# Performance work log

Measured on AMD Instinct MI355X. Metric: run time of the kernel, lower is better.

## Reference

```python
import jax, jax.numpy as jnp
import numpy as np

N_QUBITS = 10
DIM = 2 ** N_QUBITS
N_TOKENS = 32
LAYERS = 2
DEGREE = 3
VOCAB = 32000
EMB = 512
N_PARAMS = 4 * N_QUBITS * LAYERS      # angles per token circuit
N_PARAMS_FF = 4 * N_QUBITS            # quantum feedforward (1 layer)
BATCH = 32


def _ry(state, wire, theta, n):
    # state: [B, 2**n] complex64; theta: [B] float32. RY = [[c,-s],[s,c]], c=cos(th/2)
    st = state.reshape(-1, 2 ** wire, 2, 2 ** (n - wire - 1))
    c = jnp.cos(theta / 2)[:, None, None]
    s = jnp.sin(theta / 2)[:, None, None]
    a, b = st[:, :, 0, :], st[:, :, 1, :]
    st = jnp.stack([c * a - s * b, s * a + c * b], axis=2)
    return st.reshape(-1, 2 ** n)


def _crx(state, ctrl, tgt, theta, n):
    # controlled-RX: apply RX=[[c,-i s],[-i s,c]] on tgt where ctrl bit == 1
    lo, hi = (ctrl, tgt) if ctrl < tgt else (tgt, ctrl)
    st = state.reshape(-1, 2 ** lo, 2, 2 ** (hi - lo - 1), 2, 2 ** (n - hi - 1))
    caxis = 2 if ctrl < tgt else 4
    taxis = 4 if ctrl < tgt else 2
    c = jnp.cos(theta / 2).reshape(-1, 1, 1, 1, 1, 1)
    s = jnp.sin(theta / 2).reshape(-1, 1, 1, 1, 1, 1)
    c0 = jax.lax.index_in_dim(st, 0, caxis, keepdims=True)
    c1 = jax.lax.index_in_dim(st, 1, caxis, keepdims=True)
    a = jax.lax.index_in_dim(c1, 0, taxis, keepdims=True)
    b = jax.lax.index_in_dim(c1, 1, taxis, keepdims=True)
    na = c * a - 1j * s * b
    nb = -1j * s * a + c * b
    c1 = jnp.concatenate([na, nb], axis=taxis)
    st = jnp.concatenate([c0, c1], axis=caxis)
    return st.reshape(-1, 2 ** n)


def _ansatz14(state, params, n, layers):
    # gate order of ansatz 14 (arXiv:1905.10876); params: [B, 4*n*layers]
    idx = 0
    for _ in range(layers):
        for i in range(n):
            state = _ry(state, i, params[:, idx], n); idx += 1
        for i in range(n - 1, -1, -1):
            state = _crx(state, i, (i + 1) % n, params[:, idx], n); idx += 1
        for i in range(n):
            state = _ry(state, i, params[:, idx], n); idx += 1
        for i in [n - 1] + list(range(n - 1)):
            state = _crx(state, i, (i - 1) % n, params[:, idx], n); idx += 1
    return state


def _measure_xyz(state, n):
    # expectation of X,Y,Z on every wire; output [B, 3*n] ordered [x..., y..., z...]
    B = state.shape[0]
    xs, ys, zs = [], [], []
    for w in range(n):
        st = state.reshape(B, 2 ** w, 2, 2 ** (n - w - 1))
        a, b = st[:, :, 0, :], st[:, :, 1, :]
        z = jnp.sum(jnp.conj(a) * b, axis=(1, 2))
        xs.append(2.0 * jnp.real(z))
        ys.append(2.0 * jnp.imag(z))
        zs.append(jnp.sum(jnp.real(a * jnp.conj(a)) - jnp.real(b * jnp.conj(b)), axis=(1, 2)))
    return jnp.stack(xs + ys + zs, axis=1)


def _forward(x, emb, w_ang, b_ang, qsvt_coeffs, lcu_re, lcu_im, qff_params, w1, b1, w2, b2):
    B, T = x.shape
    lcu = (lcu_re + 1j * lcu_im).astype(jnp.complex64)
    lcu = lcu / jnp.maximum(jnp.sum(jnp.abs(lcu)), 1e-12)          # p=1 normalize
    angles = (emb[x] @ w_ang.T + b_ang).reshape(B * T, N_PARAMS)   # [B*T, P]
    init = jnp.zeros((B, DIM), jnp.complex64).at[:, 0].set(1.0)
    acc = qsvt_coeffs[0] * init
    mono = init
    for k in range(1, DEGREE + 1):
        rep = jnp.repeat(mono, T, axis=0)                          # [B*T, D]
        st = _ansatz14(rep, angles, N_QUBITS, LAYERS).reshape(B, T, DIM)
        mono = jnp.einsum('bwi,w->bi', st, lcu)                    # LCU combine
        acc = acc + qsvt_coeffs[k] * mono
    qsvt_state = acc / jnp.sum(jnp.abs(qsvt_coeffs))
    norm = jnp.linalg.norm(qsvt_state, axis=-1, keepdims=True)
    normed = qsvt_state / jnp.maximum(norm, 1e-12)
    qff = jnp.broadcast_to(qff_params[None, :], (B, N_PARAMS_FF))
    st2 = _ansatz14(normed, qff, N_QUBITS, 1)
    ev = _measure_xyz(st2, N_QUBITS)                               # [B, 3*nq]
    h = jax.nn.relu(ev @ w1.T + b1)
    logits = h @ w2.T + b2
    return logits, jnp.mean(norm[:, 0])


def setup_inputs() -> dict:
    key = jax.random.key(0)
    ks = jax.random.split(key, 9)
    return {
        'x': jax.random.randint(ks[0], (BATCH, N_TOKENS), 0, VOCAB, dtype=jnp.int32),
        'emb': jax.random.normal(ks[1], (VOCAB, EMB), jnp.float32) * 0.02,
        'w_ang': jax.random.normal(ks[2], (N_PARAMS, EMB), jnp.float32) * (1.0 / np.sqrt(EMB)),
        'b_ang': jnp.zeros((N_PARAMS,), jnp.float32),
        'qsvt_coeffs': jax.random.uniform(ks[3], (DEGREE + 1,), jnp.float32),
        'lcu_re': jax.random.uniform(ks[4], (N_TOKENS,), jnp.float32),
        'lcu_im': jax.random.uniform(ks[5], (N_TOKENS,), jnp.float32),
        'qff_params': jax.random.uniform(ks[6], (N_PARAMS_FF,), jnp.float32),
        'w1': jax.random.normal(ks[7], (EMB, 3 * N_QUBITS), jnp.float32) * (1.0 / np.sqrt(3 * N_QUBITS)),
        'b1': jnp.zeros((EMB,), jnp.float32),
        'w2': jax.random.normal(ks[8], (VOCAB, EMB), jnp.float32) * (1.0 / np.sqrt(EMB)),
        'b2': jnp.zeros((VOCAB,), jnp.float32),
    }


def reference(x, emb, w_ang, b_ang, qsvt_coeffs, lcu_re, lcu_im, qff_params, w1, b1, w2, b2):
    return _forward(x, emb, w_ang, b_ang, qsvt_coeffs, lcu_re, lcu_im, qff_params, w1, b1, w2, b2)
```

## Files before the change

### kernel.cpp

```cpp
#include <hip/hip_runtime.h>
#include <math.h>

#define DEV __device__ __forceinline__

namespace {

struct C2 { float x, y; };

constexpr size_t OFF_CS   = 0;
constexpr size_t OFF_NRM  = 163988;
constexpr size_t OFF_MONO = 164096;
constexpr size_t OFF_ACC  = 229632;
constexpr size_t OFF_ST   = 295168;
constexpr size_t OFF_H    = 2393280;

template<int LM>
DEV float lxor(float x) {
  if constexpr (LM == 1) {
    return __int_as_float(__builtin_amdgcn_update_dpp(
        __float_as_int(x), __float_as_int(x), 0xB1, 0xF, 0xF, false));
  } else if constexpr (LM == 2) {
    return __int_as_float(__builtin_amdgcn_update_dpp(
        __float_as_int(x), __float_as_int(x), 0x4E, 0xF, 0xF, false));
  } else if constexpr (LM == 4 || LM == 8 || LM == 16) {
    return __int_as_float(__builtin_amdgcn_ds_swizzle(
        __float_as_int(x), (LM << 10) | 0x1F));
  } else {
    return __shfl_xor(x, LM, 64);
  }
}


template<int P>
DEV void ry_gate(C2 v[16], int lane, float c, float s) {
  if constexpr (P >= 6) {
    constexpr int rm = 1 << (P - 6);
#pragma unroll
    for (int r = 0; r < 16; ++r) {
      if ((r & rm) == 0) {
        C2 a = v[r], b = v[r | rm];
        v[r].x      = fmaf(c, a.x, -s * b.x);
        v[r].y      = fmaf(c, a.y, -s * b.y);
        v[r | rm].x = fmaf(s, a.x,  c * b.x);
        v[r | rm].y = fmaf(s, a.y,  c * b.y);
      }
    }
  } else {
    constexpr int lm = 1 << P;
    float sg = (lane & lm) ? s : -s;
#pragma unroll
    for (int r = 0; r < 16; ++r) {
      float px = lxor<lm>(v[r].x);
      float py = lxor<lm>(v[r].y);
      v[r].x = fmaf(c, v[r].x, sg * px);
      v[r].y = fmaf(c, v[r].y, sg * py);
    }
  }
}

template<int PC, int PT>
DEV void crx_gate(C2 v[16], int lane, float c, float s) {
  if constexpr (PT >= 6) {
    constexpr int tm = 1 << (PT - 6);
#pragma unroll
    for (int r = 0; r < 16; ++r) {
      if ((r & tm) == 0) {
        if constexpr (PC >= 6) {
          constexpr int cm = 1 << (PC - 6);
          if ((r & cm) != 0) {
            C2 a = v[r], b = v[r | tm];
            v[r].x      = fmaf(c, a.x,  s * b.y);
            v[r].y      = fmaf(c, a.y, -s * b.x);
            v[r | tm].x = fmaf(c, b.x,  s * a.y);
            v[r | tm].y = fmaf(c, b.y, -s * a.x);
          }
        } else {
          constexpr int cl = 1 << PC;
          bool ct = (lane & cl) != 0;
          C2 a = v[r], b = v[r | tm];
          float nax = fmaf(c, a.x,  s * b.y);
          float nay = fmaf(c, a.y, -s * b.x);
          float nbx = fmaf(c, b.x,  s * a.y);
          float nby = fmaf(c, b.y, -s * a.x);
          v[r].x      = ct ? nax : a.x;
          v[r].y      = ct ? nay : a.y;
          v[r | tm].x = ct ? nbx : b.x;
          v[r | tm].y = ct ? nby : b.y;
        }
      }
    }
  } else {
    constexpr int tm = 1 << PT;
#pragma unroll
    for (int r = 0; r < 16; ++r) {
      if constexpr (PC >= 6) {
        constexpr int cm = 1 << (PC - 6);
        if ((r & cm) == 0) continue;
      }
      float px = lxor<tm>(v[r].x);
      float py = lxor<tm>(v[r].y);
      float nx = fmaf(c, v[r].x,  s * py);
      float ny = fmaf(c, v[r].y, -s * px);
      if constexpr (PC >= 6) {
        v[r].x = nx; v[r].y = ny;
      } else {
        constexpr int cl = 1 << PC;
        bool ct = (lane & cl) != 0;
        v[r].x = ct ? nx : v[r].x;
        v[r].y = ct ? ny : v[r].y;
      }
    }
  }
}

#define RYG(w, g)       ry_gate<9-(w)>(v, lane, cs[2*(g)], cs[2*(g)+1])
#define CRXG(cw, tw, g) crx_gate<9-(cw), 9-(tw)>(v, lane, cs[2*(g)], cs[2*(g)+1])

DEV void apply_layer(C2 v[16], int lane, const float* __restrict__ cs) {
  RYG(0,0); RYG(1,1); RYG(2,2); RYG(3,3); RYG(4,4);
  RYG(5,5); RYG(6,6); RYG(7,7); RYG(8,8); RYG(9,9);
  CRXG(9,0,10); CRXG(8,9,11); CRXG(7,8,12); CRXG(6,7,13); CRXG(5,6,14);
  CRXG(4,5,15); CRXG(3,4,16); CRXG(2,3,17); CRXG(1,2,18); CRXG(0,1,19);
  RYG(0,20); RYG(1,21); RYG(2,22); RYG(3,23); RYG(4,24);
  RYG(5,25); RYG(6,26); RYG(7,27); RYG(8,28); RYG(9,29);
  CRXG(9,8,30); CRXG(0,9,31); CRXG(1,0,32); CRXG(2,1,33); CRXG(3,2,34);
  CRXG(4,3,35); CRXG(5,4,36); CRXG(6,5,37); CRXG(7,6,38); CRXG(8,7,39);
}

template<int P>
DEV void measure_wire(const C2 v[16], int lane, float* ev, int w) {
  float x = 0.f, y = 0.f, z = 0.f;
  if constexpr (P >= 6) {
    constexpr int rm = 1 << (P - 6);
#pragma unroll
    for (int r = 0; r < 16; ++r) {
      if ((r & rm) == 0) {
        C2 a = v[r], b = v[r | rm];
        x += a.x*b.x + a.y*b.y;
        y += a.x*b.y - a.y*b.x;
        z += (a.x*a.x + a.y*a.y) - (b.x*b.x + b.y*b.y);
      }
    }
  } else {
    constexpr int lm = 1 << P;
#pragma unroll
    for (int r = 0; r < 16; ++r) {
      float px = lxor<lm>(v[r].x);
      float py = lxor<lm>(v[r].y);
      if ((lane & lm) == 0) {
        C2 a = v[r];
        x += a.x*px + a.y*py;
        y += a.x*py - a.y*px;
        z += (a.x*a.x + a.y*a.y) - (px*px + py*py);
      }
    }
  }
  for (int s = 1; s < 64; s <<= 1) {
    x += __shfl_xor(x, s, 64);
    y += __shfl_xor(y, s, 64);
    z += __shfl_xor(z, s, 64);
  }
  if (lane == 0) {
    ev[w]      = 2.f * x;
    ev[10 + w] = 2.f * y;
    ev[20 + w] = z;
  }
}

DEV void measure_all(const C2 v[16], int lane, float* ev) {
  measure_wire<9>(v, lane, ev, 0);
  measure_wire<8>(v, lane, ev, 1);
  measure_wire<7>(v, lane, ev, 2);
  measure_wire<6>(v, lane, ev, 3);
  measure_wire<5>(v, lane, ev, 4);
  measure_wire<4>(v, lane, ev, 5);
  measure_wire<3>(v, lane, ev, 6);
  measure_wire<2>(v, lane, ev, 7);
  measure_wire<1>(v, lane, ev, 8);
  measure_wire<0>(v, lane, ev, 9);
}


template<int K>
__global__ __launch_bounds__(256) void k_evolve(float* __restrict__ ws,
    const float* __restrict__ lr, const float* __restrict__ li,
    const int* __restrict__ x, const float* __restrict__ emb,
    const float* __restrict__ w_ang, const float* __restrict__ b_ang) {
  __shared__ float cs_lds[4][160];
  const int tid = threadIdx.x, g = blockIdx.x;
  const int wid = tid >> 6, lane = tid & 63;
  const int state = g * 4 + wid, b = state >> 5, t = state & 31;

  if constexpr (K == 1) {
    __shared__ float e4[4][512];
#pragma unroll
    for (int p = 0; p < 2; ++p) {
      int idx = tid + p * 256;
      int rr = idx >> 7, col = idx & 127;
      int row = x[g * 4 + rr];
      ((float4*)e4[rr])[col] = ((const float4*)(emb + (size_t)row * 512))[col];
    }
    __syncthreads();
#pragma unroll
    for (int p = 0; p < 2; ++p) {
      int d = tid + p * 256;
      if (d < 320) {
        int tl = d / 80, gate = d - tl * 80;
        const float4* wr = (const float4*)(w_ang + (size_t)gate * 512);
        const float4* ep = (const float4*)e4[tl];
        float a = b_ang[gate];
#pragma unroll 4
        for (int j = 0; j < 128; ++j) {
          float4 w4 = wr[j], e = ep[j];
          a = fmaf(w4.x, e.x, a); a = fmaf(w4.y, e.y, a);
          a = fmaf(w4.z, e.z, a); a = fmaf(w4.w, e.w, a);
        }
        float th = 0.5f * a, cv = cosf(th), sv = sinf(th);
        cs_lds[tl][2 * gate]     = cv;
        cs_lds[tl][2 * gate + 1] = sv;
        size_t go = OFF_CS + (size_t)(g * 4 + tl) * 160 + 2 * gate;
        ws[go] = cv; ws[go + 1] = sv;
      }
    }
    __syncthreads();
  } else {
    const float* csg = ws + OFF_CS + (size_t)g * 640;
    for (int i = tid; i < 640; i += 256) ((float*)cs_lds)[i] = csg[i];
    __syncthreads();
  }

  float lre_v = 0.f, lim_v = 0.f;
  if (lane < 32) { lre_v = lr[lane]; lim_v = li[lane]; }
  float ab = sqrtf(lre_v * lre_v + lim_v * lim_v);
  for (int s = 1; s < 64; s <<= 1) ab += __shfl_xor(ab, s, 64);
  float invL = 1.f / fmaxf(ab, 1e-12f);
  float wre = __shfl(lre_v, t, 64) * invL;
  float wim = __shfl(lim_v, t, 64) * invL;

  C2 v[16];
  if constexpr (K == 1) {
#pragma unroll
    for (int r = 0; r < 16; ++r) {
      v[r].x = (r == 0 && lane == 0) ? 1.f : 0.f;
      v[r].y = 0.f;
    }
  } else {
    const float2* mono = (const float2*)(ws + OFF_MONO) + (size_t)b * 1024;
#pragma unroll
    for (int r = 0; r < 16; ++r) {
      float2 m = mono[(r << 6) | lane];
      v[r].x = m.x; v[r].y = m.y;
    }
  }

  const float* csw = cs_lds[wid];
  apply_layer(v, lane, csw);
  apply_layer(v, lane, csw + 80);

  float2* st = (float2*)(ws + OFF_ST) + (size_t)state * 1024;
#pragma unroll
  for (int r = 0; r < 16; ++r) {
    st[(r << 6) | lane] = make_float2(wre * v[r].x - wim * v[r].y,
                                      wre * v[r].y + wim * v[r].x);
  }
}

__global__ void k_reduce(float* __restrict__ ws, const float* __restrict__ coef, int k) {
  int idx = blockIdx.x * 256 + threadIdx.x;
  int b = idx >> 10, i = idx & 1023;
  const float2* st = (const float2*)(ws + OFF_ST) + (size_t)b * 32768 + i;
  float sx = 0.f, sy = 0.f;
#pragma unroll
  for (int t = 0; t < 32; ++t) {
    float2 vv = st[t * 1024];
    sx += vv.x; sy += vv.y;
  }
  float2* mono = (float2*)(ws + OFF_MONO);
  float2* acc  = (float2*)(ws + OFF_ACC);
  float ck = coef[k];
  if (k == 1) {
    float e0 = (i == 0) ? coef[0] : 0.f;
    acc[idx] = make_float2(fmaf(ck, sx, e0), ck * sy);
    mono[idx] = make_float2(sx, sy);
  } else {
    float2 a = acc[idx];
    a.x = fmaf(ck, sx, a.x);
    a.y = fmaf(ck, sy, a.y);
    acc[idx] = a;
    mono[idx] = make_float2(sx, sy);
  }
}

__global__ __launch_bounds__(256) void k_final(float* __restrict__ ws,
                                               const float* __restrict__ coef,
                                               const float* __restrict__ qff,
                                               const float* __restrict__ w1,
                                               const float* __restrict__ b1) {
  __shared__ float qff_lds[80];
  __shared__ float2 sv[1024];
  __shared__ float ev_lds[30];
  int tid = threadIdx.x;
  int b = blockIdx.x;
  if (tid < 40) {
    float th = 0.5f * qff[tid];
    qff_lds[2 * tid]     = cosf(th);
    qff_lds[2 * tid + 1] = sinf(th);
  }
  float den = fabsf(coef[0]) + fabsf(coef[1]) + fabsf(coef[2]) + fabsf(coef[3]);
  float invd = 1.f / den;
  float c3 = coef[3];
  const float2* stb  = (const float2*)(ws + OFF_ST) + (size_t)b * 32768;
  const float2* accb = (const float2*)(ws + OFF_ACC) + (size_t)b * 1024;
#pragma unroll
  for (int q = 0; q < 4; ++q) {
    int i = tid + q * 256;
    float sx = 0.f, sy = 0.f;
#pragma unroll
    for (int t = 0; t < 32; ++t) {
      float2 vv = stb[t * 1024 + i];
      sx += vv.x; sy += vv.y;
    }
    float2 a = accb[i];
    sv[i] = make_float2(fmaf(c3, sx, a.x) * invd, fmaf(c3, sy, a.y) * invd);
  }
  __syncthreads();
  if (tid < 64) {
    int lane = tid;
    C2 v[16];
    float ssum = 0.f;
#pragma unroll
    for (int r = 0; r < 16; ++r) {
      float2 m = sv[(r << 6) | lane];
      v[r].x = m.x; v[r].y = m.y;
      ssum += v[r].x * v[r].x + v[r].y * v[r].y;
    }
    for (int s = 1; s < 64; s <<= 1) ssum += __shfl_xor(ssum, s, 64);
    float nrm = sqrtf(ssum);
    if (lane == 0) ws[OFF_NRM + b] = nrm;
    float sc = 1.f / fmaxf(nrm, 1e-12f);
#pragma unroll
    for (int r = 0; r < 16; ++r) { v[r].x *= sc; v[r].y *= sc; }
    apply_layer(v, lane, qff_lds);
    measure_all(v, lane, ev_lds);
  }
  __syncthreads();
#pragma unroll
  for (int jj = 0; jj < 2; ++jj) {
    int j = tid + jj * 256;
    const float* wr = w1 + (size_t)j * 30;
    float a = b1[j];
#pragma unroll
    for (int q = 0; q < 30; ++q) a = fmaf(ev_lds[q], wr[q], a);
    ws[OFF_H + b * 512 + j] = fmaxf(a, 0.f);
  }
}

__global__ __launch_bounds__(256) void k_logits(const float* __restrict__ ws,
                                                const float* __restrict__ w2,
                                                const float* __restrict__ b2,
                                                float* __restrict__ out) {
  __shared__ float4 hT[4096];
  int tid = threadIdx.x;
  if (blockIdx.x == 0 && tid == 0) {
    float s = 0.f;
    for (int i = 0; i < 32; ++i) s += ws[OFF_NRM + i];
    out[32000u * 32u] = s * (1.f / 32.f);
  }
  const float4* hg = (const float4*)(ws + OFF_H);
#pragma unroll
  for (int p = 0; p < 16; ++p) {
    int idx = tid + p * 256;
    int m = idx >> 7, kf4 = idx & 127;
    hT[m * 128 + (kf4 ^ (m >> 3))] = hg[idx];
  }
  __syncthreads();

  int wv = tid >> 6, lane = tid & 63;
  int mg = lane & 3, nl = lane >> 2;
  int nbase = blockIdx.x * 64;
  float acc[4][8];
#pragma unroll
  for (int j = 0; j < 4; ++j)
#pragma unroll
    for (int mi = 0; mi < 8; ++mi) acc[j][mi] = 0.f;

  const float* wbase = w2 + (size_t)(nbase + nl * 4) * 512 + wv * 128;
  int kqb = wv * 32;
#pragma unroll 2
  for (int kf4 = 0; kf4 < 32; ++kf4) {
    int kcol = kqb + kf4;
    float4 h4[8];
#pragma unroll
    for (int mi = 0; mi < 8; ++mi) {
      int m = mg * 8 + mi;
      h4[mi] = hT[m * 128 + (kcol ^ mg)];
    }
#pragma unroll
    for (int j = 0; j < 4; ++j) {
      float4 w4 = *(const float4*)(wbase + (size_t)j * 512 + kf4 * 4);
#pragma unroll
      for (int mi = 0; mi < 8; ++mi) {
        acc[j][mi] = fmaf(w4.x, h4[mi].x, acc[j][mi]);
        acc[j][mi] = fmaf(w4.y, h4[mi].y, acc[j][mi]);
        acc[j][mi] = fmaf(w4.z, h4[mi].z, acc[j][mi]);
        acc[j][mi] = fmaf(w4.w, h4[mi].w, acc[j][mi]);
      }
    }
  }

  __syncthreads();
#pragma unroll
  for (int mi = 0; mi < 8; ++mi) {
    hT[wv * 512 + lane * 8 + (mi ^ (lane & 7))] =
        make_float4(acc[0][mi], acc[1][mi], acc[2][mi], acc[3][mi]);
  }
  __syncthreads();
  {
    int lane2 = tid & 63, grp = tid >> 6;
    int mg2 = lane2 & 3, nl2 = lane2 >> 2;
#pragma unroll
    for (int jj = 0; jj < 2; ++jj) {
      int mi2 = grp * 2 + jj;
      float4 s0 = hT[0 * 512 + lane2 * 8 + (mi2 ^ (lane2 & 7))];
      float4 s1 = hT[1 * 512 + lane2 * 8 + (mi2 ^ (lane2 & 7))];
      float4 s2 = hT[2 * 512 + lane2 * 8 + (mi2 ^ (lane2 & 7))];
      float4 s3 = hT[3 * 512 + lane2 * 8 + (mi2 ^ (lane2 & 7))];
      float sx = s0.x + s1.x + s2.x + s3.x;
      float sy = s0.y + s1.y + s2.y + s3.y;
      float sz = s0.z + s1.z + s2.z + s3.z;
      float sw = s0.w + s1.w + s2.w + s3.w;
      int m = mg2 * 8 + mi2;
      int col = nbase + nl2 * 4;
      float4 b2v = *(const float4*)(b2 + col);
      float4 res = make_float4(sx + b2v.x, sy + b2v.y, sz + b2v.z, sw + b2v.w);
      *(float4*)(out + (size_t)m * 32000 + col) = res;
    }
  }
}

}

extern "C" void kernel_launch(void* const* d_in, const int* in_sizes, int n_in,
                              void* d_out, int out_size, void* d_ws, size_t ws_size,
                              hipStream_t stream) {
  (void)in_sizes; (void)n_in; (void)out_size; (void)ws_size;
  const int*   x    = (const int*)d_in[0];
  const float* emb  = (const float*)d_in[1];
  const float* wang = (const float*)d_in[2];
  const float* bang = (const float*)d_in[3];
  const float* coef = (const float*)d_in[4];
  const float* lre  = (const float*)d_in[5];
  const float* lim  = (const float*)d_in[6];
  const float* qff  = (const float*)d_in[7];
  const float* w1   = (const float*)d_in[8];
  const float* b1   = (const float*)d_in[9];
  const float* w2   = (const float*)d_in[10];
  const float* b2   = (const float*)d_in[11];
  float* out = (float*)d_out;
  float* ws  = (float*)d_ws;

  hipLaunchKernelGGL(k_evolve<1>, dim3(256), dim3(256), 0, stream,
                     ws, lre, lim, x, emb, wang, bang);
  hipLaunchKernelGGL(k_reduce, dim3(128), dim3(256), 0, stream, ws, coef, 1);
  hipLaunchKernelGGL(k_evolve<2>, dim3(256), dim3(256), 0, stream,
                     ws, lre, lim, x, emb, wang, bang);
  hipLaunchKernelGGL(k_reduce, dim3(128), dim3(256), 0, stream, ws, coef, 2);
  hipLaunchKernelGGL(k_evolve<3>, dim3(256), dim3(256), 0, stream,
                     ws, lre, lim, x, emb, wang, bang);
  hipLaunchKernelGGL(k_final,  dim3(32),  dim3(256), 0, stream, ws, coef, qff, w1, b1);
  hipLaunchKernelGGL(k_logits, dim3(500), dim3(256), 0, stream, ws, w2, b2, out);
}
```

Before: 149.0 us.

## Evolve two batch states per wavefront to interleave independent gate chains

Each wavefront now holds two statevectors (batch b and b+16 for the same token) and applies every RY and CRX gate to both in lockstep. The aim is instruction-level parallelism, so the latency of cross-lane shuffles and dependent FMA chains is hidden by independent work. Blocks shrink to 128 threads, and the shared buffer is enlarged and aliased to hold the embeddings and angles for four states. Register use per thread roughly doubles, so occupancy may fall, and the total number of waves drops by half.

```diff
diff --git a/kernel.cpp b/kernel.cpp
--- a/kernel.cpp
+++ b/kernel.cpp
@@ -29,7 +29,6 @@
     return __shfl_xor(x, LM, 64);
   }
 }
-
 
 template<int P>
 DEV void ry_gate(C2 v[16], int lane, float c, float s) {
@@ -181,33 +180,162 @@
 }
 
 
+template<int P>
+DEV void ry2(C2 va[16], C2 vb[16], int lane,
+             float ca, float sa, float cb, float sb) {
+  if constexpr (P >= 6) {
+    constexpr int rm = 1 << (P - 6);
+#pragma unroll
+    for (int r = 0; r < 16; ++r) {
+      if ((r & rm) == 0) {
+        C2 a0 = va[r], a1 = va[r | rm];
+        C2 b0 = vb[r], b1 = vb[r | rm];
+        va[r].x      = fmaf(ca, a0.x, -sa * a1.x);
+        va[r].y      = fmaf(ca, a0.y, -sa * a1.y);
+        va[r | rm].x = fmaf(sa, a0.x,  ca * a1.x);
+        va[r | rm].y = fmaf(sa, a0.y,  ca * a1.y);
+        vb[r].x      = fmaf(cb, b0.x, -sb * b1.x);
+        vb[r].y      = fmaf(cb, b0.y, -sb * b1.y);
+        vb[r | rm].x = fmaf(sb, b0.x,  cb * b1.x);
+        vb[r | rm].y = fmaf(sb, b0.y,  cb * b1.y);
+      }
+    }
+  } else {
+    constexpr int lm = 1 << P;
+    float sga = (lane & lm) ? sa : -sa;
+    float sgb = (lane & lm) ? sb : -sb;
+#pragma unroll
+    for (int r = 0; r < 16; ++r) {
+      float pax = lxor<lm>(va[r].x), pay = lxor<lm>(va[r].y);
+      float pbx = lxor<lm>(vb[r].x), pby = lxor<lm>(vb[r].y);
+      va[r].x = fmaf(ca, va[r].x, sga * pax);
+      va[r].y = fmaf(ca, va[r].y, sga * pay);
+      vb[r].x = fmaf(cb, vb[r].x, sgb * pbx);
+      vb[r].y = fmaf(cb, vb[r].y, sgb * pby);
+    }
+  }
+}
+
+template<int PC, int PT>
+DEV void crx2(C2 va[16], C2 vb[16], int lane,
+              float ca, float sa, float cb, float sb) {
+  if constexpr (PT >= 6) {
+    constexpr int tm = 1 << (PT - 6);
+#pragma unroll
+    for (int r = 0; r < 16; ++r) {
+      if ((r & tm) == 0) {
+        if constexpr (PC >= 6) {
+          constexpr int cm = 1 << (PC - 6);
+          if ((r & cm) != 0) {
+            C2 a0 = va[r], a1 = va[r | tm];
+            C2 b0 = vb[r], b1 = vb[r | tm];
+            va[r].x      = fmaf(ca, a0.x,  sa * a1.y);
+            va[r].y      = fmaf(ca, a0.y, -sa * a1.x);
+            va[r | tm].x = fmaf(ca, a1.x,  sa * a0.y);
+            va[r | tm].y = fmaf(ca, a1.y, -sa * a0.x);
+            vb[r].x      = fmaf(cb, b0.x,  sb * b1.y);
+            vb[r].y      = fmaf(cb, b0.y, -sb * b1.x);
+            vb[r | tm].x = fmaf(cb, b1.x,  sb * b0.y);
+            vb[r | tm].y = fmaf(cb, b1.y, -sb * b0.x);
+          }
+        } else {
+          constexpr int cl = 1 << PC;
+          bool ct = (lane & cl) != 0;
+          C2 a0 = va[r], a1 = va[r | tm];
+          C2 b0 = vb[r], b1 = vb[r | tm];
+          float nax = fmaf(ca, a0.x,  sa * a1.y);
+          float nay = fmaf(ca, a0.y, -sa * a1.x);
+          float nbx = fmaf(ca, a1.x,  sa * a0.y);
+          float nby = fmaf(ca, a1.y, -sa * a0.x);
+          va[r].x      = ct ? nax : a0.x;
+          va[r].y      = ct ? nay : a0.y;
+          va[r | tm].x = ct ? nbx : a1.x;
+          va[r | tm].y = ct ? nby : a1.y;
+          float mbx0 = fmaf(cb, b0.x,  sb * b1.y);
+          float mby0 = fmaf(cb, b0.y, -sb * b1.x);
+          float mbx1 = fmaf(cb, b1.x,  sb * b0.y);
+          float mby1 = fmaf(cb, b1.y, -sb * b0.x);
+          vb[r].x      = ct ? mbx0 : b0.x;
+          vb[r].y      = ct ? mby0 : b0.y;
+          vb[r | tm].x = ct ? mbx1 : b1.x;
+          vb[r | tm].y = ct ? mby1 : b1.y;
+        }
+      }
+    }
+  } else {
+    constexpr int tm = 1 << PT;
+#pragma unroll
+    for (int r = 0; r < 16; ++r) {
+      if constexpr (PC >= 6) {
+        constexpr int cm = 1 << (PC - 6);
+        if ((r & cm) == 0) continue;
+      }
+      float pax = lxor<tm>(va[r].x), pay = lxor<tm>(va[r].y);
+      float pbx = lxor<tm>(vb[r].x), pby = lxor<tm>(vb[r].y);
+      float nax = fmaf(ca, va[r].x,  sa * pay);
+      float nay = fmaf(ca, va[r].y, -sa * pax);
+      float nbx = fmaf(cb, vb[r].x,  sb * pby);
+      float nby = fmaf(cb, vb[r].y, -sb * pbx);
+      if constexpr (PC >= 6) {
+        va[r].x = nax; va[r].y = nay;
+        vb[r].x = nbx; vb[r].y = nby;
+      } else {
+        constexpr int cl = 1 << PC;
+        bool ct = (lane & cl) != 0;
+        va[r].x = ct ? nax : va[r].x;
+        va[r].y = ct ? nay : va[r].y;
+        vb[r].x = ct ? nbx : vb[r].x;
+        vb[r].y = ct ? nby : vb[r].y;
+      }
+    }
+  }
+}
+
+#define RYG2(w, g)  ry2<9-(w)>(va, vb, lane, csA[2*(g)], csA[2*(g)+1], csB[2*(g)], csB[2*(g)+1])
+#define CRXG2(cw, tw, g) crx2<9-(cw), 9-(tw)>(va, vb, lane, csA[2*(g)], csA[2*(g)+1], csB[2*(g)], csB[2*(g)+1])
+
+DEV void apply_layer2(C2 va[16], C2 vb[16], int lane,
+                      const float* __restrict__ csA, const float* __restrict__ csB) {
+  RYG2(0,0); RYG2(1,1); RYG2(2,2); RYG2(3,3); RYG2(4,4);
+  RYG2(5,5); RYG2(6,6); RYG2(7,7); RYG2(8,8); RYG2(9,9);
+  CRXG2(9,0,10); CRXG2(8,9,11); CRXG2(7,8,12); CRXG2(6,7,13); CRXG2(5,6,14);
+  CRXG2(4,5,15); CRXG2(3,4,16); CRXG2(2,3,17); CRXG2(1,2,18); CRXG2(0,1,19);
+  RYG2(0,20); RYG2(1,21); RYG2(2,22); RYG2(3,23); RYG2(4,24);
+  RYG2(5,25); RYG2(6,26); RYG2(7,27); RYG2(8,28); RYG2(9,29);
+  CRXG2(9,8,30); CRXG2(0,9,31); CRXG2(1,0,32); CRXG2(2,1,33); CRXG2(3,2,34);
+  CRXG2(4,3,35); CRXG2(5,4,36); CRXG2(6,5,37); CRXG2(7,6,38); CRXG2(8,7,39);
+}
+
+
 template<int K>
-__global__ __launch_bounds__(256) void k_evolve(float* __restrict__ ws,
+__global__ __launch_bounds__(128) void k_evolve(float* __restrict__ ws,
     const float* __restrict__ lr, const float* __restrict__ li,
     const int* __restrict__ x, const float* __restrict__ emb,
     const float* __restrict__ w_ang, const float* __restrict__ b_ang) {
-  __shared__ float cs_lds[4][160];
+  __shared__ float big[21504];
+  float (*cs_lds)[160] = (float (*)[160])big;
+  float* e4 = big + 640;
   const int tid = threadIdx.x, g = blockIdx.x;
   const int wid = tid >> 6, lane = tid & 63;
-  const int state = g * 4 + wid, b = state >> 5, t = state & 31;
+  const int s = g * 2 + wid;
+  const int t = s & 31, bp = s >> 5;
 
   if constexpr (K == 1) {
-    __shared__ float e4[4][512];
-#pragma unroll
-    for (int p = 0; p < 2; ++p) {
-      int idx = tid + p * 256;
-      int rr = idx >> 7, col = idx & 127;
-      int row = x[g * 4 + rr];
-      ((float4*)e4[rr])[col] = ((const float4*)(emb + (size_t)row * 512))[col];
+#pragma unroll
+    for (int q = 0; q < 4; ++q) {
+      int sq = g * 2 + (q >> 1);
+      int bq = (sq >> 5) + (q & 1) * 16;
+      int row = x[bq * 32 + (sq & 31)];
+      ((float4*)(e4 + q * 512))[tid] = ((const float4*)(emb + (size_t)row * 512))[tid];
     }
     __syncthreads();
 #pragma unroll
-    for (int p = 0; p < 2; ++p) {
-      int d = tid + p * 256;
+    for (int p = 0; p < 3; ++p) {
+      int d = tid + p * 128;
       if (d < 320) {
-        int tl = d / 80, gate = d - tl * 80;
+        int q = d / 80, gate = d - q * 80;
         const float4* wr = (const float4*)(w_ang + (size_t)gate * 512);
-        const float4* ep = (const float4*)e4[tl];
+        const float4* ep = (const float4*)(e4 + q * 512);
         float a = b_ang[gate];
 #pragma unroll 4
         for (int j = 0; j < 128; ++j) {
@@ -216,52 +344,67 @@
           a = fmaf(w4.z, e.z, a); a = fmaf(w4.w, e.w, a);
         }
         float th = 0.5f * a, cv = cosf(th), sv = sinf(th);
-        cs_lds[tl][2 * gate]     = cv;
-        cs_lds[tl][2 * gate + 1] = sv;
-        size_t go = OFF_CS + (size_t)(g * 4 + tl) * 160 + 2 * gate;
+        cs_lds[q][2 * gate]     = cv;
+        cs_lds[q][2 * gate + 1] = sv;
+        int sq = g * 2 + (q >> 1);
+        int bq = (sq >> 5) + (q & 1) * 16;
+        size_t go = OFF_CS + (size_t)(bq * 32 + (sq & 31)) * 160 + 2 * gate;
         ws[go] = cv; ws[go + 1] = sv;
       }
     }
     __syncthreads();
   } else {
-    const float* csg = ws + OFF_CS + (size_t)g * 640;
-    for (int i = tid; i < 640; i += 256) ((float*)cs_lds)[i] = csg[i];
+#pragma unroll
+    for (int q = 0; q < 4; ++q) {
+      int sq = g * 2 + (q >> 1);
+      int bq = (sq >> 5) + (q & 1) * 16;
+      const float* csg = ws + OFF_CS + (size_t)(bq * 32 + (sq & 31)) * 160;
+      for (int i = tid; i < 160; i += 128) cs_lds[q][i] = csg[i];
+    }
     __syncthreads();
   }
 
   float lre_v = 0.f, lim_v = 0.f;
   if (lane < 32) { lre_v = lr[lane]; lim_v = li[lane]; }
   float ab = sqrtf(lre_v * lre_v + lim_v * lim_v);
-  for (int s = 1; s < 64; s <<= 1) ab += __shfl_xor(ab, s, 64);
+  for (int ss = 1; ss < 64; ss <<= 1) ab += __shfl_xor(ab, ss, 64);
   float invL = 1.f / fmaxf(ab, 1e-12f);
   float wre = __shfl(lre_v, t, 64) * invL;
   float wim = __shfl(lim_v, t, 64) * invL;
 
-  C2 v[16];
+  C2 va[16], vb[16];
   if constexpr (K == 1) {
 #pragma unroll
     for (int r = 0; r < 16; ++r) {
-      v[r].x = (r == 0 && lane == 0) ? 1.f : 0.f;
-      v[r].y = 0.f;
-    }
-  } else {
-    const float2* mono = (const float2*)(ws + OFF_MONO) + (size_t)b * 1024;
-#pragma unroll
-    for (int r = 0; r < 16; ++r) {
-      float2 m = mono[(r << 6) | lane];
-      v[r].x = m.x; v[r].y = m.y;
-    }
-  }
-
-  const float* csw = cs_lds[wid];
-  apply_layer(v, lane, csw);
-  apply_layer(v, lane, csw + 80);
-
-  float2* st = (float2*)(ws + OFF_ST) + (size_t)state * 1024;
+      float init = (r == 0 && lane == 0) ? 1.f : 0.f;
+      va[r].x = init; va[r].y = 0.f;
+      vb[r].x = init; vb[r].y = 0.f;
+    }
+  } else {
+    const float2* monoA = (const float2*)(ws + OFF_MONO) + (size_t)bp * 1024;
+    const float2* monoB = (const float2*)(ws + OFF_MONO) + (size_t)(bp + 16) * 1024;
+#pragma unroll
+    for (int r = 0; r < 16; ++r) {
+      float2 ma = monoA[(r << 6) | lane];
+      float2 mb = monoB[(r << 6) | lane];
+      va[r].x = ma.x; va[r].y = ma.y;
+      vb[r].x = mb.x; vb[r].y = mb.y;
+    }
+  }
+
+  const float* csA = cs_lds[wid * 2 + 0];
+  const float* csB = cs_lds[wid * 2 + 1];
+  apply_layer2(va, vb, lane, csA, csB);
+  apply_layer2(va, vb, lane, csA + 80, csB + 80);
+
+  float2* stA = (float2*)(ws + OFF_ST) + (size_t)(bp * 32 + t) * 1024;
+  float2* stB = (float2*)(ws + OFF_ST) + (size_t)((bp + 16) * 32 + t) * 1024;
 #pragma unroll
   for (int r = 0; r < 16; ++r) {
-    st[(r << 6) | lane] = make_float2(wre * v[r].x - wim * v[r].y,
-                                      wre * v[r].y + wim * v[r].x);
+    stA[(r << 6) | lane] = make_float2(wre * va[r].x - wim * va[r].y,
+                                       wre * va[r].y + wim * va[r].x);
+    stB[(r << 6) | lane] = make_float2(wre * vb[r].x - wim * vb[r].y,
+                                       wre * vb[r].y + wim * vb[r].x);
   }
 }
 
@@ -459,13 +602,13 @@
   float* out = (float*)d_out;
   float* ws  = (float*)d_ws;
 
-  hipLaunchKernelGGL(k_evolve<1>, dim3(256), dim3(256), 0, stream,
+  hipLaunchKernelGGL(k_evolve<1>, dim3(256), dim3(128), 0, stream,
                      ws, lre, lim, x, emb, wang, bang);
   hipLaunchKernelGGL(k_reduce, dim3(128), dim3(256), 0, stream, ws, coef, 1);
-  hipLaunchKernelGGL(k_evolve<2>, dim3(256), dim3(256), 0, stream,
+  hipLaunchKernelGGL(k_evolve<2>, dim3(256), dim3(128), 0, stream,
                      ws, lre, lim, x, emb, wang, bang);
   hipLaunchKernelGGL(k_reduce, dim3(128), dim3(256), 0, stream, ws, coef, 2);
-  hipLaunchKernelGGL(k_evolve<3>, dim3(256), dim3(256), 0, stream,
+  hipLaunchKernelGGL(k_evolve<3>, dim3(256), dim3(128), 0, stream,
                      ws, lre, lim, x, emb, wang, bang);
   hipLaunchKernelGGL(k_final,  dim3(32),  dim3(256), 0, stream, ws, coef, qff, w1, b1);
   hipLaunchKernelGGL(k_logits, dim3(500), dim3(256), 0, stream, ws, w2, b2, out);
```

New measurement: 189.9 us. +27.4%, slower.
